# Optimization experiments

Measured on AMD Instinct MI355X. Metric: run time of the kernel, lower is better.

The kernel has to match this reference:

```python
import jax, jax.numpy as jnp
import numpy as np
import math

B, N, D_MODEL, H, D_HEAD = 2, 2048, 1024, 16, 64
EPS = 1e-6

def setup_inputs() -> dict:
    key = jax.random.key(0)
    ks = jax.random.split(key, 6)
    s = 1.0 / math.sqrt(D_MODEL)
    return {
        "X": jax.random.normal(ks[0], (B, N, D_MODEL), dtype=jnp.float32),
        "Wq": jax.random.normal(ks[1], (D_MODEL, H * D_HEAD), dtype=jnp.float32) * s,
        "Wk": jax.random.normal(ks[2], (D_MODEL, H * D_HEAD), dtype=jnp.float32) * s,
        "Wv": jax.random.normal(ks[3], (D_MODEL, H * D_HEAD), dtype=jnp.float32) * s,
        "Wo": jax.random.normal(ks[4], (H * D_HEAD, D_MODEL), dtype=jnp.float32) * s,
        "bo": jnp.zeros((D_MODEL,), dtype=jnp.float32),
    }

def reference(X, Wq, Wk, Wv, Wo, bo):
    b, n, _ = X.shape
    # project and split heads -> [b, h, n, d_head]
    def heads(Y):
        return Y.reshape(b, n, H, D_HEAD).transpose(0, 2, 1, 3)
    Q = heads(X @ Wq)
    K = heads(X @ Wk)
    V = heads(X @ Wv)
    # per-head L2 normalization of Q and K
    Q = Q / (jnp.linalg.norm(Q, axis=-1, keepdims=True) + EPS)
    K = K / (jnp.linalg.norm(K, axis=-1, keepdims=True) + EPS)
    # scores [b, h, n, n]
    A = jnp.einsum("bhqd,bhkd->bhqk", Q, K) / math.sqrt(D_HEAD)
    causal = jnp.triu(jnp.ones((n, n), dtype=bool), k=1)
    A = jnp.where(causal, -jnp.inf, A)
    A = jax.nn.softmax(A, axis=-1)
    V_hat = jnp.einsum("bhqk,bhkd->bhqd", A, V)
    V_hat = V_hat.transpose(0, 2, 1, 3).reshape(b, n, H * D_HEAD)
    return V_hat @ Wo + bo
```

## Files before the change

kernel.cpp:

```cpp
#include <hip/hip_runtime.h>
#include <hip/hip_bf16.h>
#include <math.h>

#define BATCH 2
#define NSEQ  2048
#define DM    1024
#define NH    16
#define DH    64
#define EPS_N 1e-6f

typedef unsigned short u16;
typedef __attribute__((ext_vector_type(8))) short short8;
typedef __attribute__((ext_vector_type(8))) unsigned short u16x8;
typedef __attribute__((ext_vector_type(4))) unsigned short u16x4;
typedef __attribute__((ext_vector_type(4))) float f32x4;

__device__ __forceinline__ u16 f2bf(float x) {
  __hip_bfloat16 h = __float2bfloat16(x);
  return *reinterpret_cast<u16*>(&h);
}

__device__ __forceinline__ void gl_lds16(const u16* g, u16* lds_base) {
  __builtin_amdgcn_global_load_lds(
      (__attribute__((address_space(1))) void*)g,
      (__attribute__((address_space(3))) void*)lds_base, 16, 0, 0);
}

__global__ __launch_bounds__(256) void prep(
    const float* __restrict__ X,
    const float* __restrict__ w0, const float* __restrict__ w1,
    const float* __restrict__ w2, const float* __restrict__ w3,
    u16* __restrict__ Xb, u16* __restrict__ WT) {
  const int id = blockIdx.x, tid = threadIdx.x;
  if (id >= 1024) {
    size_t base = ((size_t)(id - 1024) * 256 + tid) * 8;
    float4 f0 = *(const float4*)&X[base];
    float4 f1 = *(const float4*)&X[base + 4];
    u16x8 v;
    v[0] = f2bf(f0.x); v[1] = f2bf(f0.y); v[2] = f2bf(f0.z); v[3] = f2bf(f0.w);
    v[4] = f2bf(f1.x); v[5] = f2bf(f1.y); v[6] = f2bf(f1.z); v[7] = f2bf(f1.w);
    *(u16x8*)&Xb[base] = v;
    return;
  }
  const int z = id >> 8, xy = id & 255, bx = xy & 15, by = xy >> 4;
  const float* in = (z == 0) ? w0 : (z == 1) ? w1 : (z == 2) ? w2 : w3;
  u16* o = WT + (size_t)z * DM * DM;
  __shared__ u16 T[64][65];
  const int n0 = bx * 64, k0 = by * 64;
  #pragma unroll
  for (int i = 0; i < 4; i++) {
    int c = tid + 256 * i, row = c >> 4, col4 = c & 15;
    float4 f = *(const float4*)&in[(size_t)(k0 + row) * DM + n0 + col4 * 4];
    T[row][col4 * 4 + 0] = f2bf(f.x);
    T[row][col4 * 4 + 1] = f2bf(f.y);
    T[row][col4 * 4 + 2] = f2bf(f.z);
    T[row][col4 * 4 + 3] = f2bf(f.w);
  }
  __syncthreads();
  #pragma unroll
  for (int i = 0; i < 2; i++) {
    int c = tid + 256 * i, row = c >> 3, col8 = c & 7;
    u16x8 v;
    #pragma unroll
    for (int e = 0; e < 8; e++) v[e] = T[col8 * 8 + e][row];
    *(u16x8*)&o[(size_t)(n0 + row) * DM + k0 + col8 * 8] = v;
  }
}

#define GEMM128_MAINLOOP(Aptr, Btptr)                                          \
  __shared__ u16 As[128 * 64];                                                 \
  __shared__ u16 Bs[128 * 64];                                                 \
  const int tid = threadIdx.x, w = tid >> 6, lane = tid & 63;                  \
  const int ml = lane & 15, quad = lane >> 4;                                  \
  const int m0 = blockIdx.y * 128, n0 = blockIdx.x * 128;                      \
  const int wm = w & 1, wn = w >> 1;                                           \
  const int srow = lane >> 3;                      \
  const int scol = ((lane & 7) ^ srow) * 8;         \
  f32x4 acc[4][4];                                                             \
  _Pragma("unroll") for (int mi = 0; mi < 4; mi++)                             \
    _Pragma("unroll") for (int ni = 0; ni < 4; ni++)                           \
      _Pragma("unroll") for (int e = 0; e < 4; e++) acc[mi][ni][e] = 0.f;      \
  for (int k0 = 0; k0 < DM; k0 += 64) {                                        \
    __syncthreads();                                                           \
    _Pragma("unroll") for (int L = 0; L < 4; L++) {                            \
      int I = w * 4 + L;                                                       \
      gl_lds16(Aptr  + (size_t)(m0 + I * 8 + srow) * DM + k0 + scol,           \
               As + I * 512);                                                  \
      gl_lds16(Btptr + (size_t)(n0 + I * 8 + srow) * DM + k0 + scol,           \
               Bs + I * 512);                                                  \
    }                                                                          \
    __syncthreads();                                                           \
    _Pragma("unroll") for (int kk = 0; kk < 64; kk += 32) {                    \
      const int kc = kk >> 3;                          \
      short8 am[4], bn[4];                                                     \
      _Pragma("unroll") for (int i = 0; i < 4; i++) {                          \
        int ra = wm * 64 + i * 16 + ml;                                        \
        int rb = wn * 64 + i * 16 + ml;                                        \
        am[i] = *(const short8*)&As[ra * 64 + (((quad + kc) ^ (ra & 7)) * 8)]; \
        bn[i] = *(const short8*)&Bs[rb * 64 + (((quad + kc) ^ (rb & 7)) * 8)]; \
      }                                                                        \
      _Pragma("unroll") for (int mi = 0; mi < 4; mi++)                         \
        _Pragma("unroll") for (int ni = 0; ni < 4; ni++)                       \
          acc[mi][ni] = __builtin_amdgcn_mfma_f32_16x16x32_bf16(               \
              am[mi], bn[ni], acc[mi][ni], 0, 0, 0);                           \
    }                                                                          \
  }

__global__ __launch_bounds__(256) void gemm_qkv128(
    const u16* __restrict__ Xb, const u16* __restrict__ WT,
    u16* __restrict__ Qo, u16* __restrict__ Ko, u16* __restrict__ Vt) {
  const u16* Bt = WT + (size_t)blockIdx.z * DM * DM;
  GEMM128_MAINLOOP(Xb, Bt)
  const int z = blockIdx.z;
  if (z < 2) {
    u16* OutQK = (z == 0) ? Qo : Ko;
    const float qsc = (z == 0) ? 0.125f * 1.44269504f : 1.0f;
    const int h = (n0 >> 6) + wn;
    #pragma unroll
    for (int mi = 0; mi < 4; mi++) {
      int mrow0 = m0 + wm * 64 + mi * 16 + quad * 4;
      int b = mrow0 >> 11, tok0 = mrow0 & (NSEQ - 1);
      #pragma unroll
      for (int r = 0; r < 4; r++) {
        float ss = 0.f;
        #pragma unroll
        for (int ni = 0; ni < 4; ni++) ss += acc[mi][ni][r] * acc[mi][ni][r];
        ss += __shfl_xor(ss, 1, 64);
        ss += __shfl_xor(ss, 2, 64);
        ss += __shfl_xor(ss, 4, 64);
        ss += __shfl_xor(ss, 8, 64);
        float sc = qsc / (sqrtf(ss) + EPS_N);
        #pragma unroll
        for (int ni = 0; ni < 4; ni++)
          OutQK[((size_t)(b * NH + h) * NSEQ + tok0 + r) * DH + ni * 16 + ml] =
              f2bf(acc[mi][ni][r] * sc);
      }
    }
  } else {
    #pragma unroll
    for (int mi = 0; mi < 4; mi++) {
      int mrow0 = m0 + wm * 64 + mi * 16 + quad * 4;
      int b = mrow0 >> 11, tok0 = mrow0 & (NSEQ - 1);
      #pragma unroll
      for (int ni = 0; ni < 4; ni++) {
        int n = n0 + wn * 64 + ni * 16 + ml;
        int h = n >> 6, d = n & 63;
        u16x4 pk;
        #pragma unroll
        for (int r = 0; r < 4; r++) pk[r] = f2bf(acc[mi][ni][r]);
        *(u16x4*)&Vt[((size_t)(b * NH + h) * DH + d) * NSEQ + tok0] = pk;
      }
    }
  }
}

__global__ __launch_bounds__(256) void gemm_proj128(
    const u16* __restrict__ A, const u16* __restrict__ BtW,
    const float* __restrict__ bias, float* __restrict__ out) {
  GEMM128_MAINLOOP(A, BtW)
  #pragma unroll
  for (int ni = 0; ni < 4; ni++) {
    int n = n0 + wn * 64 + ni * 16 + ml;
    float bz = bias[n];
    #pragma unroll
    for (int mi = 0; mi < 4; mi++) {
      int mrow0 = m0 + wm * 64 + mi * 16 + quad * 4;
      #pragma unroll
      for (int r = 0; r < 4; r++)
        out[(size_t)(mrow0 + r) * DM + n] = acc[mi][ni][r] + bz;
    }
  }
}

__global__ __launch_bounds__(256) void flash_attn(
    const u16* __restrict__ Qb, const u16* __restrict__ Kb,
    const u16* __restrict__ Vt, u16* __restrict__ vhat) {
  const int tid = threadIdx.x, w = tid >> 6, lane = tid & 63;
  const int ml = lane & 15, quad = lane >> 4;
  const int bh = blockIdx.x;
  const int bb = bh >> 4, hb = bh & 15;
  const u16* Qh = Qb + (size_t)bh * NSEQ * DH;
  const u16* Kh = Kb + (size_t)bh * NSEQ * DH;
  const u16* Vth = Vt + (size_t)bh * DH * NSEQ;

  __shared__ u16 Ks [64 * 64];
  __shared__ u16 VsT[64 * 64];
  __shared__ u16 Ps [4][32][76];

  const int srow = lane >> 3;
  const int scol = ((lane & 7) ^ srow) * 8;

  for (int ph = 0; ph < 2; ph++) {
    const int qblk = ph ? (int)blockIdx.y : (15 - (int)blockIdx.y);
    const int q0 = qblk * 128;
    const int ntiles = 2 * (qblk + 1);

    short8 aq[2][2];
    #pragma unroll
    for (int m = 0; m < 2; m++)
      #pragma unroll
      for (int c = 0; c < 2; c++)
        aq[m][c] = *(const short8*)
            &Qh[(size_t)(q0 + w * 32 + m * 16 + ml) * DH + c * 32 + quad * 8];

    f32x4 oacc[2][4];
    #pragma unroll
    for (int m = 0; m < 2; m++)
      #pragma unroll
      for (int n = 0; n < 4; n++)
        #pragma unroll
        for (int e = 0; e < 4; e++) oacc[m][n][e] = 0.f;
    float l_[2][4] = {{0.f, 0.f, 0.f, 0.f}, {0.f, 0.f, 0.f, 0.f}};

    for (int t = 0; t < ntiles; t++) {
      const int j0 = t * 64;
      __syncthreads();
      #pragma unroll
      for (int i2 = 0; i2 < 2; i2++) {
        int i = w + 4 * i2;
        gl_lds16(Kh  + (size_t)(j0 + i * 8 + srow) * DH + scol, Ks  + i * 512);
        gl_lds16(Vth + (size_t)(i * 8 + srow) * NSEQ + j0 + scol, VsT + i * 512);
      }
      __syncthreads();

      f32x4 sacc[2][4];
      #pragma unroll
      for (int m = 0; m < 2; m++)
        #pragma unroll
        for (int n = 0; n < 4; n++)
          #pragma unroll
          for (int e = 0; e < 4; e++) sacc[m][n][e] = 0.f;
      #pragma unroll
      for (int c = 0; c < 2; c++)
        #pragma unroll
        for (int n = 0; n < 4; n++) {
          int rk = n * 16 + ml;
          short8 kf = *(const short8*)
              &Ks[rk * 64 + (((c * 4 + quad) ^ (rk & 7)) * 8)];
          #pragma unroll
          for (int m = 0; m < 2; m++)
            sacc[m][n] = __builtin_amdgcn_mfma_f32_16x16x32_bf16(
                aq[m][c], kf, sacc[m][n], 0, 0, 0);
        }

      #pragma unroll
      for (int m = 0; m < 2; m++)
        #pragma unroll
        for (int n = 0; n < 4; n++) {
          int j = j0 + n * 16 + ml;
          #pragma unroll
          for (int r = 0; r < 4; r++) {
            int q = q0 + w * 32 + m * 16 + quad * 4 + r;
            float e = __builtin_amdgcn_exp2f(sacc[m][n][r]);
            e = (j > q) ? 0.f : e;
            l_[m][r] += e;
            Ps[w][m * 16 + quad * 4 + r][n * 16 + ml] = f2bf(e);
          }
        }

      #pragma unroll
      for (int c = 0; c < 2; c++) {
        short8 ap[2];
        #pragma unroll
        for (int m = 0; m < 2; m++)
          ap[m] = *(const short8*)&Ps[w][m * 16 + ml][c * 32 + quad * 8];
        #pragma unroll
        for (int n = 0; n < 4; n++) {
          int rv = n * 16 + ml;
          short8 bv = *(const short8*)
              &VsT[rv * 64 + (((c * 4 + quad) ^ (rv & 7)) * 8)];
          #pragma unroll
          for (int m = 0; m < 2; m++)
            oacc[m][n] = __builtin_amdgcn_mfma_f32_16x16x32_bf16(
                ap[m], bv, oacc[m][n], 0, 0, 0);
        }
      }
    }

    #pragma unroll
    for (int m = 0; m < 2; m++)
      #pragma unroll
      for (int r = 0; r < 4; r++) {
        float lv = l_[m][r];
        lv += __shfl_xor(lv, 1, 64);
        lv += __shfl_xor(lv, 2, 64);
        lv += __shfl_xor(lv, 4, 64);
        lv += __shfl_xor(lv, 8, 64);
        float inv = 1.f / lv;
        int q = q0 + w * 32 + m * 16 + quad * 4 + r;
        #pragma unroll
        for (int n = 0; n < 4; n++)
          vhat[((size_t)(bb * NSEQ + q)) * DM + hb * DH + n * 16 + ml] =
              f2bf(oacc[m][n][r] * inv);
      }
  }
}

extern "C" void kernel_launch(void* const* d_in, const int* in_sizes, int n_in,
                              void* d_out, int out_size, void* d_ws, size_t ws_size,
                              hipStream_t stream) {
  const float* X  = (const float*)d_in[0];
  const float* Wq = (const float*)d_in[1];
  const float* Wk = (const float*)d_in[2];
  const float* Wv = (const float*)d_in[3];
  const float* Wo = (const float*)d_in[4];
  const float* bo = (const float*)d_in[5];
  float* out = (float*)d_out;

  const size_t NE = (size_t)BATCH * NSEQ * DM;
  u16* Qb   = (u16*)d_ws;
  u16* Kb   = Qb + NE;
  u16* Vt   = Kb + NE;
  u16* XbVh = Vt + NE;
  u16* WT   = XbVh + NE;

  prep        <<<dim3(3072),      256, 0, stream>>>(X, Wq, Wk, Wv, Wo, XbVh, WT);
  gemm_qkv128 <<<dim3(8, 32, 3),  256, 0, stream>>>(XbVh, WT, Qb, Kb, Vt);
  flash_attn  <<<dim3(32, 8),     256, 0, stream>>>(Qb, Kb, Vt, XbVh);
  gemm_proj128<<<dim3(8, 32, 1),  256, 0, stream>>>(XbVh, WT + 3 * (size_t)DM * DM,
                                                    bo, out);
}
```

Before: 214.8 us.

## Double-buffer K/V tiles, compute softmax row sums with MFMA, mask only diagonal tiles

```diff
diff --git a/kernel.cpp b/kernel.cpp
--- a/kernel.cpp
+++ b/kernel.cpp
@@ -183,12 +183,16 @@
   const u16* Kh = Kb + (size_t)bh * NSEQ * DH;
   const u16* Vth = Vt + (size_t)bh * DH * NSEQ;
 
-  __shared__ u16 Ks [64 * 64];
-  __shared__ u16 VsT[64 * 64];
+  __shared__ u16 Ks [2][64 * 64];
+  __shared__ u16 VsT[2][64 * 64];
   __shared__ u16 Ps [4][32][76];
 
   const int srow = lane >> 3;
   const int scol = ((lane & 7) ^ srow) * 8;
+
+  short8 ones;
+  #pragma unroll
+  for (int e = 0; e < 8; e++) ones[e] = (short)0x3F80;
 
   for (int ph = 0; ph < 2; ph++) {
     const int qblk = ph ? (int)blockIdx.y : (15 - (int)blockIdx.y);
@@ -203,25 +207,41 @@
         aq[m][c] = *(const short8*)
             &Qh[(size_t)(q0 + w * 32 + m * 16 + ml) * DH + c * 32 + quad * 8];
 
-    f32x4 oacc[2][4];
-    #pragma unroll
-    for (int m = 0; m < 2; m++)
+    f32x4 oacc[2][4], lacc[2];
+    #pragma unroll
+    for (int m = 0; m < 2; m++) {
       #pragma unroll
       for (int n = 0; n < 4; n++)
         #pragma unroll
         for (int e = 0; e < 4; e++) oacc[m][n][e] = 0.f;
-    float l_[2][4] = {{0.f, 0.f, 0.f, 0.f}, {0.f, 0.f, 0.f, 0.f}};
+      #pragma unroll
+      for (int e = 0; e < 4; e++) lacc[m][e] = 0.f;
+    }
+
+    __syncthreads();
+    #pragma unroll
+    for (int i2 = 0; i2 < 2; i2++) {
+      int i = w + 4 * i2;
+      gl_lds16(Kh  + (size_t)(i * 8 + srow) * DH + scol, Ks[0]  + i * 512);
+      gl_lds16(Vth + (size_t)(i * 8 + srow) * NSEQ + scol, VsT[0] + i * 512);
+    }
 
     for (int t = 0; t < ntiles; t++) {
+      __syncthreads();
+      if (t + 1 < ntiles) {
+        const int j1 = (t + 1) * 64;
+        #pragma unroll
+        for (int i2 = 0; i2 < 2; i2++) {
+          int i = w + 4 * i2;
+          gl_lds16(Kh  + (size_t)(j1 + i * 8 + srow) * DH + scol,
+                   Ks[(t + 1) & 1] + i * 512);
+          gl_lds16(Vth + (size_t)(i * 8 + srow) * NSEQ + j1 + scol,
+                   VsT[(t + 1) & 1] + i * 512);
+        }
+      }
+      const u16* KsC  = Ks[t & 1];
+      const u16* VsTC = VsT[t & 1];
       const int j0 = t * 64;
-      __syncthreads();
-      #pragma unroll
-      for (int i2 = 0; i2 < 2; i2++) {
-        int i = w + 4 * i2;
-        gl_lds16(Kh  + (size_t)(j0 + i * 8 + srow) * DH + scol, Ks  + i * 512);
-        gl_lds16(Vth + (size_t)(i * 8 + srow) * NSEQ + j0 + scol, VsT + i * 512);
-      }
-      __syncthreads();
 
       f32x4 sacc[2][4];
       #pragma unroll
@@ -236,27 +256,37 @@
         for (int n = 0; n < 4; n++) {
           int rk = n * 16 + ml;
           short8 kf = *(const short8*)
-              &Ks[rk * 64 + (((c * 4 + quad) ^ (rk & 7)) * 8)];
+              &KsC[rk * 64 + (((c * 4 + quad) ^ (rk & 7)) * 8)];
           #pragma unroll
           for (int m = 0; m < 2; m++)
             sacc[m][n] = __builtin_amdgcn_mfma_f32_16x16x32_bf16(
                 aq[m][c], kf, sacc[m][n], 0, 0, 0);
         }
 
-      #pragma unroll
-      for (int m = 0; m < 2; m++)
-        #pragma unroll
-        for (int n = 0; n < 4; n++) {
-          int j = j0 + n * 16 + ml;
-          #pragma unroll
-          for (int r = 0; r < 4; r++) {
-            int q = q0 + w * 32 + m * 16 + quad * 4 + r;
-            float e = __builtin_amdgcn_exp2f(sacc[m][n][r]);
-            e = (j > q) ? 0.f : e;
-            l_[m][r] += e;
-            Ps[w][m * 16 + quad * 4 + r][n * 16 + ml] = f2bf(e);
+      if (t >= ntiles - 2) {
+        #pragma unroll
+        for (int m = 0; m < 2; m++)
+          #pragma unroll
+          for (int n = 0; n < 4; n++) {
+            int j = j0 + n * 16 + ml;
+            #pragma unroll
+            for (int r = 0; r < 4; r++) {
+              int q = q0 + w * 32 + m * 16 + quad * 4 + r;
+              float e = __builtin_amdgcn_exp2f(sacc[m][n][r]);
+              e = (j > q) ? 0.f : e;
+              Ps[w][m * 16 + quad * 4 + r][n * 16 + ml] = f2bf(e);
+            }
           }
-        }
+      } else {
+        #pragma unroll
+        for (int m = 0; m < 2; m++)
+          #pragma unroll
+          for (int n = 0; n < 4; n++)
+            #pragma unroll
+            for (int r = 0; r < 4; r++)
+              Ps[w][m * 16 + quad * 4 + r][n * 16 + ml] =
+                  f2bf(__builtin_amdgcn_exp2f(sacc[m][n][r]));
+      }
 
       #pragma unroll
       for (int c = 0; c < 2; c++) {
@@ -264,11 +294,15 @@
         #pragma unroll
         for (int m = 0; m < 2; m++)
           ap[m] = *(const short8*)&Ps[w][m * 16 + ml][c * 32 + quad * 8];
+        #pragma unroll
+        for (int m = 0; m < 2; m++)
+          lacc[m] = __builtin_amdgcn_mfma_f32_16x16x32_bf16(
+              ap[m], ones, lacc[m], 0, 0, 0);
         #pragma unroll
         for (int n = 0; n < 4; n++) {
           int rv = n * 16 + ml;
           short8 bv = *(const short8*)
-              &VsT[rv * 64 + (((c * 4 + quad) ^ (rv & 7)) * 8)];
+              &VsTC[rv * 64 + (((c * 4 + quad) ^ (rv & 7)) * 8)];
           #pragma unroll
           for (int m = 0; m < 2; m++)
             oacc[m][n] = __builtin_amdgcn_mfma_f32_16x16x32_bf16(
@@ -281,12 +315,7 @@
     for (int m = 0; m < 2; m++)
       #pragma unroll
       for (int r = 0; r < 4; r++) {
-        float lv = l_[m][r];
-        lv += __shfl_xor(lv, 1, 64);
-        lv += __shfl_xor(lv, 2, 64);
-        lv += __shfl_xor(lv, 4, 64);
-        lv += __shfl_xor(lv, 8, 64);
-        float inv = 1.f / lv;
+        float inv = 1.f / lacc[m][r];
         int q = q0 + w * 32 + m * 16 + quad * 4 + r;
         #pragma unroll
         for (int n = 0; n < 4; n++)
```

New measurement: 207.2 us. -3.5%, faster.
